# Kernel optimization log

Hardware: AMD Instinct MI355X
Metric: run time of the kernel (lower is better)

## Reference

```python
import math
import jax, jax.numpy as jnp
import numpy as np

B, S, D_IN = 2, 2048, 1024
DKQ, DV, H = 1024, 1024, 16
HEAD_SIZE = DKQ / H  # attention_head_size (float division, as in torch)


def setup_inputs() -> dict:
    key = jax.random.key(0)
    k1, k2, k3, k4, k5, k6 = jax.random.split(key, 6)
    std = 1.0 / math.sqrt(D_IN)
    return {
        'hidden_states': jax.random.normal(k1, (B, S, D_IN), dtype=jnp.float32),
        'Wq': jax.random.normal(k2, (DKQ, D_IN), dtype=jnp.float32) * std,
        'Wk': jax.random.normal(k3, (DKQ, D_IN), dtype=jnp.float32) * std,
        'Wv': jax.random.normal(k4, (DV, D_IN), dtype=jnp.float32) * std,
        'bv': jax.random.normal(k5, (DV,), dtype=jnp.float32) * std,
        'mixing': jax.random.normal(k6, (H, DKQ), dtype=jnp.float32) * 0.2,  # UNIFORM init: normal(std=0.2)
    }


def reference(hidden_states, Wq, Wk, Wv, bv, mixing):
    # Q, K: [B, S, DKQ]; V: [B, S, DV]
    q = jnp.einsum('bsd,ed->bse', hidden_states, Wq)
    k = jnp.einsum('bsd,ed->bse', hidden_states, Wk)
    v = jnp.einsum('bsd,ed->bse', hidden_states, Wv) + bv
    # per-head query mixing: mixed_q[b,h,s,e] = q[b,s,e] * mixing[h,e]
    # scores[b,h,s,t] = sum_e mixed_q[b,h,s,e] * k[b,t,e]
    scores = jnp.einsum('bse,he,bte->bhst', q, mixing, k)
    scores = scores / math.sqrt(HEAD_SIZE)
    probs = jax.nn.softmax(scores, axis=-1)
    # value heads: [B, H, S, DV/H]
    v_h = v.reshape(v.shape[0], v.shape[1], H, DV // H).transpose(0, 2, 1, 3)
    ctx = jnp.einsum('bhst,bhtd->bhsd', probs, v_h)
    # back to [B, S, DV]
    ctx = ctx.transpose(0, 2, 1, 3).reshape(hidden_states.shape[0], hidden_states.shape[1], DV)
    return ctx
```

## Files before the change

### kernel.cpp

```cpp
#include <hip/hip_runtime.h>

#define B_ 2
#define S_ 2048
#define D_ 1024
#define H_ 16
#define HD_ 64

typedef _Float16 f16;
typedef _Float16 half8 __attribute__((ext_vector_type(8)));
typedef float float4_ __attribute__((ext_vector_type(4)));

#define N_HS (B_*S_*D_)
#define N_W  (D_*D_)
#define N_MIX (H_*D_)

__device__ __forceinline__ void gl_lds16(const f16* g, const f16* l) {
  __builtin_amdgcn_global_load_lds(
      (const __attribute__((address_space(1))) void*)g,
      (__attribute__((address_space(3))) void*)l, 16, 0, 0);
}

#define MIX_SCALE 0.18033688011112042f

__global__ __launch_bounds__(256) void convert_kernel(
    const float* __restrict__ hs, const float* __restrict__ wq,
    const float* __restrict__ wk, const float* __restrict__ wv,
    const float* __restrict__ mix,
    f16* __restrict__ hs16, f16* __restrict__ wq16, f16* __restrict__ wk16,
    f16* __restrict__ wv16, f16* __restrict__ mix16)
{
  const int total4 = (N_HS + 3*N_W + N_MIX) / 4;
  for (int i4 = blockIdx.x*blockDim.x + threadIdx.x; i4 < total4;
       i4 += gridDim.x*blockDim.x) {
    int i = i4*4;
    const float* src; f16* dst; float scale = 1.0f; int off;
    if (i < N_HS)            { src=hs;  dst=hs16;  off=i; }
    else if (i < N_HS+N_W)   { src=wq;  dst=wq16;  off=i-N_HS; }
    else if (i < N_HS+2*N_W) { src=wk;  dst=wk16;  off=i-N_HS-N_W; }
    else if (i < N_HS+3*N_W) { src=wv;  dst=wv16;  off=i-N_HS-2*N_W; }
    else                     { src=mix; dst=mix16; off=i-N_HS-3*N_W; scale=MIX_SCALE; }
    float4 v = *(const float4*)(src+off);
    dst[off]   = (f16)(v.x*scale);
    dst[off+1] = (f16)(v.y*scale);
    dst[off+2] = (f16)(v.z*scale);
    dst[off+3] = (f16)(v.w*scale);
  }
}

#define BM 128
#define BN 128
#define BK 64
#define LDA 72

__global__ __launch_bounds__(256, 2) void qkv_kernel(
    const f16* __restrict__ hs16, const f16* __restrict__ w16base,
    const float* __restrict__ bv,
    f16* __restrict__ q16, f16* __restrict__ k16, f16* __restrict__ vT)
{
  const int z = blockIdx.z;
  const f16* W = w16base + (size_t)z * N_W;
  f16* out = (z==0) ? q16 : k16;
  const int mt = blockIdx.y, nt = blockIdx.x;
  const int tid = threadIdx.x;
  const int lane = tid & 63, wid = tid >> 6;
  const int wm = wid >> 1, wn = wid & 1;
  const int quad = lane >> 4, l16 = lane & 15;

  __shared__ __align__(16) f16 As[BM][LDA];
  __shared__ __align__(16) f16 Bs[BN][LDA];

  float4_ acc[4][4];
#pragma unroll
  for (int i=0;i<4;i++)
#pragma unroll
    for (int j=0;j<4;j++) acc[i][j] = (float4_)0.0f;

  const int row0 = mt*BM;
  const int col0 = nt*BN;

  for (int ko = 0; ko < D_; ko += BK) {
#pragma unroll
    for (int it=0; it<4; it++) {
      int c = it*256 + tid;
      int r = c >> 3, c8 = (c & 7)*8;
      *(half8*)&As[r][c8] = *(const half8*)&hs16[(size_t)(row0+r)*D_ + ko + c8];
      *(half8*)&Bs[r][c8] = *(const half8*)&W[(size_t)(col0+r)*D_ + ko + c8];
    }
    __syncthreads();
#pragma unroll
    for (int kk=0; kk<BK; kk+=32) {
      half8 a[4], b[4];
#pragma unroll
      for (int i=0;i<4;i++) a[i] = *(const half8*)&As[wm*64+i*16+l16][kk+quad*8];
#pragma unroll
      for (int j=0;j<4;j++) b[j] = *(const half8*)&Bs[wn*64+j*16+l16][kk+quad*8];
#pragma unroll
      for (int i=0;i<4;i++)
#pragma unroll
        for (int j=0;j<4;j++)
          acc[i][j] = __builtin_amdgcn_mfma_f32_16x16x32_f16(a[i], b[j], acc[i][j], 0,0,0);
    }
    __syncthreads();
  }
#pragma unroll
  for (int i=0;i<4;i++) {
#pragma unroll
    for (int j=0;j<4;j++) {
      int colg = col0 + wn*64 + j*16 + l16;
      float bias = (z==2) ? bv[colg] : 0.0f;
#pragma unroll
      for (int r=0;r<4;r++) {
        int rowg = row0 + wm*64 + i*16 + quad*4 + r;
        f16 val = (f16)(acc[i][j][r] + bias);
        if (z == 2) {
          int bb = rowg >> 11, ss = rowg & (S_-1);
          vT[((size_t)bb*D_ + colg)*S_ + ss] = val;
        } else {
          out[(size_t)rowg*D_ + colg] = val;
        }
      }
    }
  }
}

#define TQ 128
#define TK 128
#define LDP 136
#define CSHIFT2 4.328085122666891f

__global__ __launch_bounds__(256, 2) void attn_kernel(
    const f16* __restrict__ q16, const f16* __restrict__ k16,
    const f16* __restrict__ vT, const f16* __restrict__ mix16,
    float* __restrict__ out)
{
  const int b = blockIdx.z;
  const int h = blockIdx.y;
  const int s0 = blockIdx.x * TQ;
  const int tid = threadIdx.x;
  const int lane = tid & 63, wid = tid >> 6;
  const int wm = wid >> 1, wn = wid & 1;
  const int quad = lane >> 4, l16 = lane & 15;

  __shared__ __align__(16) union {
    struct { f16 q[TQ][LDA]; f16 k0[TK*BK]; f16 k1[TK*BK]; } s1;
    f16 P[TQ][LDP];
  } u;
  __shared__ __align__(16) float red_l[2][TQ];

  float l_lane[16];
#pragma unroll
  for (int t=0;t<16;t++) l_lane[t] = 0.0f;

  float4_ o_acc[4][2];
#pragma unroll
  for (int i=0;i<4;i++)
#pragma unroll
    for (int j=0;j<2;j++) o_acc[i][j] = (float4_)0.0f;

  const f16* qbase = q16 + (size_t)(b*S_ + s0)*D_;
  const f16* kbase = k16 + (size_t)b*S_*D_;
  const f16* mrow  = mix16 + h*D_;
  const f16* vTb   = vT + (size_t)(b*D_ + h*HD_)*S_;

  for (int t0 = 0; t0 < S_; t0 += 2*TK) {
    float4_ sacc[2][4][4];
#pragma unroll
    for (int tt=0;tt<2;tt++)
#pragma unroll
      for (int i=0;i<4;i++)
#pragma unroll
        for (int j=0;j<4;j++) sacc[tt][i][j] = (float4_)0.0f;

    for (int ko = 0; ko < D_; ko += BK) {
      const f16* k0g = kbase + (size_t)t0*D_ + ko;
      const f16* k1g = k0g + (size_t)TK*D_;
#pragma unroll
      for (int c=0; c<4; c++) {
        int slot = (wid*4+c)*64 + lane;
        int r = slot >> 3;
        int gc = (slot & 7) ^ (r & 7);
        gl_lds16(k0g + (size_t)r*D_ + gc*8, u.s1.k0 + (size_t)(wid*4+c)*64*8);
        gl_lds16(k1g + (size_t)r*D_ + gc*8, u.s1.k1 + (size_t)(wid*4+c)*64*8);
      }
#pragma unroll
      for (int it=0; it<4; it++) {
        int c = it*256 + tid;
        int r = c >> 3, c8 = (c & 7)*8;
        half8 qv = *(const half8*)&qbase[(size_t)r*D_ + ko + c8];
        half8 mv = *(const half8*)&mrow[ko + c8];
        *(half8*)&u.s1.q[r][c8] = qv * mv;
      }
      __syncthreads();
#pragma unroll
      for (int kk=0; kk<BK; kk+=32) {
        half8 a[4];
#pragma unroll
        for (int i=0;i<4;i++) a[i] = *(const half8*)&u.s1.q[wm*64+i*16+l16][kk+quad*8];
#pragma unroll
        for (int tt=0;tt<2;tt++) {
          const f16* kb = tt ? u.s1.k1 : u.s1.k0;
          half8 bf[4];
#pragma unroll
          for (int j=0;j<4;j++) {
            int rr = wn*64 + j*16 + l16;
            int ck = (kk >> 3) + quad;
            bf[j] = *(const half8*)&kb[(size_t)(((rr<<3) | (ck ^ (rr&7))) << 3)];
          }
#pragma unroll
          for (int i=0;i<4;i++)
#pragma unroll
            for (int j=0;j<4;j++)
              sacc[tt][i][j] = __builtin_amdgcn_mfma_f32_16x16x32_f16(a[i], bf[j], sacc[tt][i][j], 0,0,0);
        }
      }
      __syncthreads();
    }

#pragma unroll
    for (int tt=0;tt<2;tt++) {
#pragma unroll
      for (int i=0;i<4;i++)
#pragma unroll
        for (int j=0;j<4;j++)
#pragma unroll
          for (int r=0;r<4;r++) {
            float p = __builtin_exp2f(sacc[tt][i][j][r] - CSHIFT2);
            l_lane[i*4+r] += p;
            u.P[wm*64+i*16+quad*4+r][wn*64+j*16+l16] = (f16)p;
          }

      half8 vb[8];
#pragma unroll
      for (int ki=0; ki<4; ki++)
#pragma unroll
        for (int j=0; j<2; j++) {
          int ch = wn*32 + j*16 + l16;
          vb[ki*2+j] = *(const half8*)&vTb[(size_t)ch*S_ + t0 + tt*TK + ki*32 + quad*8];
        }

      __syncthreads();

#pragma unroll
      for (int ki=0; ki<4; ki++) {
        half8 pa[4];
#pragma unroll
        for (int i=0;i<4;i++) pa[i] = *(const half8*)&u.P[wm*64+i*16+l16][ki*32+quad*8];
#pragma unroll
        for (int i=0;i<4;i++)
#pragma unroll
          for (int j=0;j<2;j++)
            o_acc[i][j] = __builtin_amdgcn_mfma_f32_16x16x32_f16(pa[i], vb[ki*2+j], o_acc[i][j], 0,0,0);
      }
      __syncthreads();
    }
  }

#pragma unroll
  for (int d=1; d<16; d<<=1)
#pragma unroll
    for (int t=0;t<16;t++) l_lane[t] += __shfl_xor(l_lane[t], d);
  if (l16 == 0) {
#pragma unroll
    for (int i=0;i<4;i++)
#pragma unroll
      for (int r=0;r<4;r++)
        red_l[wn][wm*64+i*16+quad*4+r] = l_lane[i*4+r];
  }
  __syncthreads();

#pragma unroll
  for (int i=0;i<4;i++) {
#pragma unroll
    for (int r=0;r<4;r++) {
      int row = wm*64 + i*16 + quad*4 + r;
      float linv = 1.0f / (red_l[0][row] + red_l[1][row]);
#pragma unroll
      for (int j=0;j<2;j++) {
        int colg = h*HD_ + wn*32 + j*16 + l16;
        out[(size_t)(b*S_ + s0 + row)*D_ + colg] = o_acc[i][j][r] * linv;
      }
    }
  }
}

extern "C" void kernel_launch(void* const* d_in, const int* in_sizes, int n_in,
                              void* d_out, int out_size, void* d_ws, size_t ws_size,
                              hipStream_t stream) {
  (void)in_sizes; (void)n_in; (void)out_size; (void)ws_size;
  const float* hs  = (const float*)d_in[0];
  const float* Wq  = (const float*)d_in[1];
  const float* Wk  = (const float*)d_in[2];
  const float* Wv  = (const float*)d_in[3];
  const float* bv  = (const float*)d_in[4];
  const float* mix = (const float*)d_in[5];
  float* out = (float*)d_out;

  char* ws = (char*)d_ws;
  f16* hs16  = (f16*)(ws);
  f16* w16   = (f16*)(ws + 8388608);
  f16* mix16 = (f16*)(ws + 14680064);
  f16* q16   = (f16*)(ws + 14712832);
  f16* k16   = (f16*)(ws + 23101440);
  f16* vT    = (f16*)(ws + 31490048);

  convert_kernel<<<2048, 256, 0, stream>>>(hs, Wq, Wk, Wv, mix,
                                           hs16, w16, w16+N_W, w16+2*N_W, mix16);
  qkv_kernel<<<dim3(D_/BN, (B_*S_)/BM, 3), 256, 0, stream>>>(
      hs16, w16, bv, q16, k16, vT);
  attn_kernel<<<dim3(S_/TQ, H_, B_), 256, 0, stream>>>(
      q16, k16, vT, mix16, out);
}
```

Before: 437.5 us.

## Fuse fp32-to-fp16 conversion into QKV GEMM loads and cache mixing row in LDS

Removes the separate conversion kernel. The QKV GEMM now reads fp32 hidden states and weights directly and converts them to fp16 while filling shared memory, and one block also converts the mixing matrix. The attention kernel stages its head's mixing row in LDS. It also drops the constant softmax shift and issues the V loads before the exp/P-store loop. This saves one launch and the fp16 intermediate writes and reads, but each GEMM tile re-reads fp32 inputs at twice the bytes. Without the shift, unshifted exp2 values stored as fp16 have less headroom before overflow.

After: 529.0 us. +20.9%, slower.

```diff
diff --git a/kernel.cpp b/kernel.cpp
--- a/kernel.cpp
+++ b/kernel.cpp
@@ -10,9 +10,10 @@
 typedef _Float16 half8 __attribute__((ext_vector_type(8)));
 typedef float float4_ __attribute__((ext_vector_type(4)));
 
-#define N_HS (B_*S_*D_)
 #define N_W  (D_*D_)
 #define N_MIX (H_*D_)
+
+#define MIX_SCALE 0.18033688011112042f
 
 __device__ __forceinline__ void gl_lds16(const f16* g, const f16* l) {
   __builtin_amdgcn_global_load_lds(
@@ -20,31 +21,12 @@
       (__attribute__((address_space(3))) void*)l, 16, 0, 0);
 }
 
-#define MIX_SCALE 0.18033688011112042f
-
-__global__ __launch_bounds__(256) void convert_kernel(
-    const float* __restrict__ hs, const float* __restrict__ wq,
-    const float* __restrict__ wk, const float* __restrict__ wv,
-    const float* __restrict__ mix,
-    f16* __restrict__ hs16, f16* __restrict__ wq16, f16* __restrict__ wk16,
-    f16* __restrict__ wv16, f16* __restrict__ mix16)
-{
-  const int total4 = (N_HS + 3*N_W + N_MIX) / 4;
-  for (int i4 = blockIdx.x*blockDim.x + threadIdx.x; i4 < total4;
-       i4 += gridDim.x*blockDim.x) {
-    int i = i4*4;
-    const float* src; f16* dst; float scale = 1.0f; int off;
-    if (i < N_HS)            { src=hs;  dst=hs16;  off=i; }
-    else if (i < N_HS+N_W)   { src=wq;  dst=wq16;  off=i-N_HS; }
-    else if (i < N_HS+2*N_W) { src=wk;  dst=wk16;  off=i-N_HS-N_W; }
-    else if (i < N_HS+3*N_W) { src=wv;  dst=wv16;  off=i-N_HS-2*N_W; }
-    else                     { src=mix; dst=mix16; off=i-N_HS-3*N_W; scale=MIX_SCALE; }
-    float4 v = *(const float4*)(src+off);
-    dst[off]   = (f16)(v.x*scale);
-    dst[off+1] = (f16)(v.y*scale);
-    dst[off+2] = (f16)(v.z*scale);
-    dst[off+3] = (f16)(v.w*scale);
-  }
+__device__ __forceinline__ half8 cvt8(const float* p) {
+  float4 a0 = *(const float4*)p, a1 = *(const float4*)(p+4);
+  half8 h;
+  h[0]=(f16)a0.x; h[1]=(f16)a0.y; h[2]=(f16)a0.z; h[3]=(f16)a0.w;
+  h[4]=(f16)a1.x; h[5]=(f16)a1.y; h[6]=(f16)a1.z; h[7]=(f16)a1.w;
+  return h;
 }
 
 #define BM 128
@@ -53,12 +35,14 @@
 #define LDA 72
 
 __global__ __launch_bounds__(256, 2) void qkv_kernel(
-    const f16* __restrict__ hs16, const f16* __restrict__ w16base,
-    const float* __restrict__ bv,
-    f16* __restrict__ q16, f16* __restrict__ k16, f16* __restrict__ vT)
+    const float* __restrict__ hs, const float* __restrict__ Wq,
+    const float* __restrict__ Wk, const float* __restrict__ Wv,
+    const float* __restrict__ bv, const float* __restrict__ mix,
+    f16* __restrict__ q16, f16* __restrict__ k16, f16* __restrict__ vT,
+    f16* __restrict__ mix16)
 {
   const int z = blockIdx.z;
-  const f16* W = w16base + (size_t)z * N_W;
+  const float* W = (z==0) ? Wq : (z==1) ? Wk : Wv;
   f16* out = (z==0) ? q16 : k16;
   const int mt = blockIdx.y, nt = blockIdx.x;
   const int tid = threadIdx.x;
@@ -66,6 +50,20 @@
   const int wm = wid >> 1, wn = wid & 1;
   const int quad = lane >> 4, l16 = lane & 15;
 
+  if (z == 0 && mt == 0 && nt == 0) {
+#pragma unroll
+    for (int i = 0; i < 8; i++) {
+      int e = (i*256 + tid) * 8;
+      float4 a0 = *(const float4*)&mix[e], a1 = *(const float4*)&mix[e+4];
+      half8 h;
+      h[0]=(f16)(a0.x*MIX_SCALE); h[1]=(f16)(a0.y*MIX_SCALE);
+      h[2]=(f16)(a0.z*MIX_SCALE); h[3]=(f16)(a0.w*MIX_SCALE);
+      h[4]=(f16)(a1.x*MIX_SCALE); h[5]=(f16)(a1.y*MIX_SCALE);
+      h[6]=(f16)(a1.z*MIX_SCALE); h[7]=(f16)(a1.w*MIX_SCALE);
+      *(half8*)&mix16[e] = h;
+    }
+  }
+
   __shared__ __align__(16) f16 As[BM][LDA];
   __shared__ __align__(16) f16 Bs[BN][LDA];
 
@@ -83,8 +81,8 @@
     for (int it=0; it<4; it++) {
       int c = it*256 + tid;
       int r = c >> 3, c8 = (c & 7)*8;
-      *(half8*)&As[r][c8] = *(const half8*)&hs16[(size_t)(row0+r)*D_ + ko + c8];
-      *(half8*)&Bs[r][c8] = *(const half8*)&W[(size_t)(col0+r)*D_ + ko + c8];
+      *(half8*)&As[r][c8] = cvt8(&hs[(size_t)(row0+r)*D_ + ko + c8]);
+      *(half8*)&Bs[r][c8] = cvt8(&W[(size_t)(col0+r)*D_ + ko + c8]);
     }
     __syncthreads();
 #pragma unroll
@@ -126,7 +124,6 @@
 #define TQ 128
 #define TK 128
 #define LDP 136
-#define CSHIFT2 4.328085122666891f
 
 __global__ __launch_bounds__(256, 2) void attn_kernel(
     const f16* __restrict__ q16, const f16* __restrict__ k16,
@@ -145,6 +142,7 @@
     struct { f16 q[TQ][LDA]; f16 k0[TK*BK]; f16 k1[TK*BK]; } s1;
     f16 P[TQ][LDP];
   } u;
+  __shared__ __align__(16) f16 mixrow[D_];
   __shared__ __align__(16) float red_l[2][TQ];
 
   float l_lane[16];
@@ -159,8 +157,10 @@
 
   const f16* qbase = q16 + (size_t)(b*S_ + s0)*D_;
   const f16* kbase = k16 + (size_t)b*S_*D_;
-  const f16* mrow  = mix16 + h*D_;
   const f16* vTb   = vT + (size_t)(b*D_ + h*HD_)*S_;
+
+  if (tid < D_/8) *(half8*)&mixrow[tid*8] = *(const half8*)&mix16[h*D_ + tid*8];
+  __syncthreads();
 
   for (int t0 = 0; t0 < S_; t0 += 2*TK) {
     float4_ sacc[2][4][4];
@@ -187,7 +187,7 @@
         int c = it*256 + tid;
         int r = c >> 3, c8 = (c & 7)*8;
         half8 qv = *(const half8*)&qbase[(size_t)r*D_ + ko + c8];
-        half8 mv = *(const half8*)&mrow[ko + c8];
+        half8 mv = *(const half8*)&mixrow[ko + c8];
         *(half8*)&u.s1.q[r][c8] = qv * mv;
       }
       __syncthreads();
@@ -218,17 +218,6 @@
 
 #pragma unroll
     for (int tt=0;tt<2;tt++) {
-#pragma unroll
-      for (int i=0;i<4;i++)
-#pragma unroll
-        for (int j=0;j<4;j++)
-#pragma unroll
-          for (int r=0;r<4;r++) {
-            float p = __builtin_exp2f(sacc[tt][i][j][r] - CSHIFT2);
-            l_lane[i*4+r] += p;
-            u.P[wm*64+i*16+quad*4+r][wn*64+j*16+l16] = (f16)p;
-          }
-
       half8 vb[8];
 #pragma unroll
       for (int ki=0; ki<4; ki++)
@@ -237,6 +226,17 @@
           int ch = wn*32 + j*16 + l16;
           vb[ki*2+j] = *(const half8*)&vTb[(size_t)ch*S_ + t0 + tt*TK + ki*32 + quad*8];
         }
+
+#pragma unroll
+      for (int i=0;i<4;i++)
+#pragma unroll
+        for (int j=0;j<4;j++)
+#pragma unroll
+          for (int r=0;r<4;r++) {
+            float p = __builtin_exp2f(sacc[tt][i][j][r]);
+            l_lane[i*4+r] += p;
+            u.P[wm*64+i*16+quad*4+r][wn*64+j*16+l16] = (f16)p;
+          }
 
       __syncthreads();
 
@@ -296,17 +296,13 @@
   float* out = (float*)d_out;
 
   char* ws = (char*)d_ws;
-  f16* hs16  = (f16*)(ws);
-  f16* w16   = (f16*)(ws + 8388608);
-  f16* mix16 = (f16*)(ws + 14680064);
-  f16* q16   = (f16*)(ws + 14712832);
-  f16* k16   = (f16*)(ws + 23101440);
-  f16* vT    = (f16*)(ws + 31490048);
-
-  convert_kernel<<<2048, 256, 0, stream>>>(hs, Wq, Wk, Wv, mix,
-                                           hs16, w16, w16+N_W, w16+2*N_W, mix16);
+  f16* mix16 = (f16*)(ws);
+  f16* q16   = (f16*)(ws + 32768);
+  f16* k16   = (f16*)(ws + 32768 + 8388608);
+  f16* vT    = (f16*)(ws + 32768 + 16777216);
+
   qkv_kernel<<<dim3(D_/BN, (B_*S_)/BM, 3), 256, 0, stream>>>(
-      hs16, w16, bv, q16, k16, vT);
+      hs, Wq, Wk, Wv, bv, mix, q16, k16, vT, mix16);
   attn_kernel<<<dim3(S_/TQ, H_, B_), 256, 0, stream>>>(
       q16, k16, vT, mix16, out);
 }
```
